# Optimization experiments

Measured on AMD Instinct MI355X. Metric: run time of the kernel, lower is better.

The kernel has to match this reference:

```python
import jax, jax.numpy as jnp
import numpy as np

NUM_TAGS = 5
START_TAG = 3  # ent_to_ix['<START>']
STOP_TAG = 4   # ent_to_ix['<STOP>']
NEG_INF = -10000.0
B, T = 8192, 512


def setup_inputs() -> dict:
    key = jax.random.key(0)
    k1, k2 = jax.random.split(key)
    feats = jax.random.normal(k1, (B, T, NUM_TAGS), dtype=jnp.float32)
    transitions = jax.random.normal(k2, (NUM_TAGS, NUM_TAGS), dtype=jnp.float32)
    # matches __init__: no transition into START, none out of STOP
    transitions = transitions.at[START_TAG, :].set(NEG_INF)
    transitions = transitions.at[:, STOP_TAG].set(NEG_INF)
    return {"feats": feats, "transitions": transitions}


def reference(feats, transitions):
    """Batched CRF forward algorithm (log partition function).

    feats: [B, T, K] emission scores; transitions: [K, K] where
    transitions[next, prev] is the score of prev -> next.
    Returns alpha: [B] log partition per sequence.
    """
    def single(seq):  # seq: [T, K]
        init = jnp.full((NUM_TAGS,), NEG_INF, dtype=seq.dtype).at[START_TAG].set(0.0)

        def step(forward_var, feat):
            # scores[next, prev] = forward_var[prev] + transitions[next, prev] + feat[next]
            scores = forward_var[None, :] + transitions + feat[:, None]
            return jax.nn.logsumexp(scores, axis=1), None

        forward_var, _ = jax.lax.scan(step, init, seq)
        terminal = forward_var + transitions[STOP_TAG]
        return jax.nn.logsumexp(terminal)

    return jax.vmap(single)(feats)
```

## Files before the change

### kernel.cpp

```cpp
#include <hip/hip_runtime.h>

#define BB 8192
#define SEQF 2560

__device__ __forceinline__ float rfl(float x) {
    return __int_as_float(__builtin_amdgcn_readfirstlane(__float_as_int(x)));
}

__global__ __launch_bounds__(256, 4) void crf_fused(const float* __restrict__ feats,
                                                    const float* __restrict__ trans,
                                                    float* __restrict__ out) {
    const int tid  = threadIdx.x;
    const int lane = tid & 63;
    const int gw   = blockIdx.x * 4 + (tid >> 6);
    const int s0   = gw * 2;

    const float4* pA = (const float4*)(feats + (size_t)s0 * SEQF) + lane * 10;
    const float4* pB = pA + (SEQF / 4);
    float4 a0=pA[0], a1=pA[1], a2=pA[2], a3=pA[3], a4=pA[4];
    float4 a5=pA[5], a6=pA[6], a7=pA[7], a8=pA[8], a9=pA[9];
    float4 b0=pB[0], b1=pB[1], b2=pB[2], b3=pB[3], b4=pB[4];
    float4 b5=pB[5], b6=pB[6], b7=pB[7], b8=pB[8], b9=pB[9];
    __builtin_amdgcn_sched_barrier(0);

    const float E00=rfl(__expf(trans[0])),  E01=rfl(__expf(trans[1])),  E02=rfl(__expf(trans[2]));
    const float E10=rfl(__expf(trans[5])),  E11=rfl(__expf(trans[6])),  E12=rfl(__expf(trans[7]));
    const float E20=rfl(__expf(trans[10])), E21=rfl(__expf(trans[11])), E22=rfl(__expf(trans[12]));
    const float C0 =rfl(__expf(trans[3])),  C1 =rfl(__expf(trans[8])),  C2 =rfl(__expf(trans[13]));
    const float S0 =rfl(__expf(trans[20])), S1 =rfl(__expf(trans[21])), S2 =rfl(__expf(trans[22]));

#define CRF_STEP(FA, FB, FC) do {                                   \
        float e0 = __expf(FA), e1 = __expf(FB), e2 = __expf(FC);    \
        float N00 = e0 * (E00*M00 + E01*M10 + E02*M20);             \
        float N01 = e0 * (E00*M01 + E01*M11 + E02*M21);             \
        float N02 = e0 * (E00*M02 + E01*M12 + E02*M22);             \
        float N10 = e1 * (E10*M00 + E11*M10 + E12*M20);             \
        float N11 = e1 * (E10*M01 + E11*M11 + E12*M21);             \
        float N12 = e1 * (E10*M02 + E11*M12 + E12*M22);             \
        float N20 = e2 * (E20*M00 + E21*M10 + E22*M20);             \
        float N21 = e2 * (E20*M01 + E21*M11 + E22*M21);             \
        float N22 = e2 * (E20*M02 + E21*M12 + E22*M22);             \
        M00=N00; M01=N01; M02=N02;                                  \
        M10=N10; M11=N11; M12=N12;                                  \
        M20=N20; M21=N21; M22=N22;                                  \
    } while (0)

#define CRF_RENORM() do {                                           \
        float mx = fmaxf(fmaxf(fmaxf(M00,M01), fmaxf(M02,M10)),     \
                         fmaxf(fmaxf(M11,M12), fmaxf(fmaxf(M20,M21),M22))); \
        mx = fmaxf(mx, 1e-30f);                                     \
        int ee = (int)((__float_as_uint(mx) >> 23) & 0xffu) - 127;  \
        float sc = __uint_as_float((unsigned)(127 - ee) << 23);     \
        ls += (float)ee;                                            \
        M00*=sc; M01*=sc; M02*=sc;                                  \
        M10*=sc; M11*=sc; M12*=sc;                                  \
        M20*=sc; M21*=sc; M22*=sc;                                  \
    } while (0)

#define TREE_LEVEL(D) do {                                          \
        float P00=__shfl_down(M00,D), P01=__shfl_down(M01,D), P02=__shfl_down(M02,D); \
        float P10=__shfl_down(M10,D), P11=__shfl_down(M11,D), P12=__shfl_down(M12,D); \
        float P20=__shfl_down(M20,D), P21=__shfl_down(M21,D), P22=__shfl_down(M22,D); \
        float Pls=__shfl_down(ls, D);                               \
        float N00 = P00*M00 + P01*M10 + P02*M20;                    \
        float N01 = P00*M01 + P01*M11 + P02*M21;                    \
        float N02 = P00*M02 + P01*M12 + P02*M22;                    \
        float N10 = P10*M00 + P11*M10 + P12*M20;                    \
        float N11 = P10*M01 + P11*M11 + P12*M21;                    \
        float N12 = P10*M02 + P11*M12 + P12*M22;                    \
        float N20 = P20*M00 + P21*M10 + P22*M20;                    \
        float N21 = P20*M01 + P21*M11 + P22*M21;                    \
        float N22 = P20*M02 + P21*M12 + P22*M22;                    \
        M00=N00; M01=N01; M02=N02; M10=N10; M11=N11; M12=N12;       \
        M20=N20; M21=N21; M22=N22;                                  \
        ls += Pls;                                                  \
        CRF_RENORM();                                               \
    } while (0)

#define CRF_SEQ(q0,q1,q2,q3,q4,q5,q6,q7,q8,q9, OUTIDX) do {         \
        float M00, M01, M02, M10, M11, M12, M20, M21, M22;          \
        float ls = 0.0f;                                            \
        {    \
            float e0 = __expf(q0.x), e1 = __expf(q0.y), e2 = __expf(q0.z); \
            M00 = e0*E00; M01 = e0*E01; M02 = e0*E02;               \
            M10 = e1*E10; M11 = e1*E11; M12 = e1*E12;               \
            M20 = e2*E20; M21 = e2*E21; M22 = e2*E22;               \
            if (lane == 0) {                                        \
                M00 = M01 = M02 = e0*C0;                            \
                M10 = M11 = M12 = e1*C1;                            \
                M20 = M21 = M22 = e2*C2;                            \
            }                                                       \
        }                                                           \
        CRF_STEP(q1.y, q1.z, q1.w);                         \
        CRF_STEP(q2.z, q2.w, q3.x);                         \
        CRF_STEP(q3.w, q4.x, q4.y);                         \
        CRF_RENORM();                                               \
        CRF_STEP(q5.x, q5.y, q5.z);                         \
        CRF_STEP(q6.y, q6.z, q6.w);                         \
        CRF_STEP(q7.z, q7.w, q8.x);                         \
        CRF_STEP(q8.w, q9.x, q9.y);                         \
        CRF_RENORM();                                               \
        TREE_LEVEL(1);  TREE_LEVEL(2);  TREE_LEVEL(4);              \
        TREE_LEVEL(8);  TREE_LEVEL(16); TREE_LEVEL(32);             \
        float r = S0*M00 + S1*M10 + S2*M20;                         \
        float res = __logf(r) + ls * 0.69314718055994531f;          \
        if (lane == 0) out[OUTIDX] = res;                           \
    } while (0)

    CRF_SEQ(a0,a1,a2,a3,a4,a5,a6,a7,a8,a9, s0);
    CRF_SEQ(b0,b1,b2,b3,b4,b5,b6,b7,b8,b9, s0 + 1);

#undef CRF_STEP
#undef CRF_RENORM
#undef TREE_LEVEL
#undef CRF_SEQ
}

extern "C" void kernel_launch(void* const* d_in, const int* in_sizes, int n_in,
                              void* d_out, int out_size, void* d_ws, size_t ws_size,
                              hipStream_t stream) {
    const float* feats = (const float*)d_in[0];
    const float* trans = (const float*)d_in[1];
    float* out = (float*)d_out;
    (void)d_ws; (void)ws_size;

    crf_fused<<<BB / 8, 256, 0, stream>>>(feats, trans, out);
}
```

Measured before the change: 20.95 us.

## Process two sequences per wavefront with 32-lane halves and longer chunks

```diff
diff --git a/kernel.cpp b/kernel.cpp
--- a/kernel.cpp
+++ b/kernel.cpp
@@ -12,15 +12,16 @@
                                                     float* __restrict__ out) {
     const int tid  = threadIdx.x;
     const int lane = tid & 63;
+    const int half = lane >> 5;
+    const int cpos = lane & 31;
     const int gw   = blockIdx.x * 4 + (tid >> 6);
     const int s0   = gw * 2;
 
-    const float4* pA = (const float4*)(feats + (size_t)s0 * SEQF) + lane * 10;
-    const float4* pB = pA + (SEQF / 4);
-    float4 a0=pA[0], a1=pA[1], a2=pA[2], a3=pA[3], a4=pA[4];
-    float4 a5=pA[5], a6=pA[6], a7=pA[7], a8=pA[8], a9=pA[9];
-    float4 b0=pB[0], b1=pB[1], b2=pB[2], b3=pB[3], b4=pB[4];
-    float4 b5=pB[5], b6=pB[6], b7=pB[7], b8=pB[8], b9=pB[9];
+    const float4* p = (const float4*)(feats + (size_t)(s0 + half) * SEQF) + cpos * 20;
+    float4 q0 =p[0],  q1 =p[1],  q2 =p[2],  q3 =p[3],  q4 =p[4];
+    float4 q5 =p[5],  q6 =p[6],  q7 =p[7],  q8 =p[8],  q9 =p[9];
+    float4 q10=p[10], q11=p[11], q12=p[12], q13=p[13], q14=p[14];
+    float4 q15=p[15], q16=p[16], q17=p[17], q18=p[18], q19=p[19];
     __builtin_amdgcn_sched_barrier(0);
 
     const float E00=rfl(__expf(trans[0])),  E01=rfl(__expf(trans[1])),  E02=rfl(__expf(trans[2]));
@@ -28,6 +29,11 @@
     const float E20=rfl(__expf(trans[10])), E21=rfl(__expf(trans[11])), E22=rfl(__expf(trans[12]));
     const float C0 =rfl(__expf(trans[3])),  C1 =rfl(__expf(trans[8])),  C2 =rfl(__expf(trans[13]));
     const float S0 =rfl(__expf(trans[20])), S1 =rfl(__expf(trans[21])), S2 =rfl(__expf(trans[22]));
+
+    const bool c0 = (cpos == 0);
+    const float G00 = c0 ? C0 : E00, G01 = c0 ? C0 : E01, G02 = c0 ? C0 : E02;
+    const float G10 = c0 ? C1 : E10, G11 = c0 ? C1 : E11, G12 = c0 ? C1 : E12;
+    const float G20 = c0 ? C2 : E20, G21 = c0 ? C2 : E21, G22 = c0 ? C2 : E22;
 
 #define CRF_STEP(FA, FB, FC) do {                                   \
         float e0 = __expf(FA), e1 = __expf(FB), e2 = __expf(FC);    \
@@ -57,7 +63,7 @@
         M20*=sc; M21*=sc; M22*=sc;                                  \
     } while (0)
 
-#define TREE_LEVEL(D) do {                                          \
+#define TREE_LEVEL(D, RN) do {                                      \
         float P00=__shfl_down(M00,D), P01=__shfl_down(M01,D), P02=__shfl_down(M02,D); \
         float P10=__shfl_down(M10,D), P11=__shfl_down(M11,D), P12=__shfl_down(M12,D); \
         float P20=__shfl_down(M20,D), P21=__shfl_down(M21,D), P22=__shfl_down(M22,D); \
@@ -74,46 +80,49 @@
         M00=N00; M01=N01; M02=N02; M10=N10; M11=N11; M12=N12;       \
         M20=N20; M21=N21; M22=N22;                                  \
         ls += Pls;                                                  \
-        CRF_RENORM();                                               \
+        if (RN) CRF_RENORM();                                       \
     } while (0)
 
-#define CRF_SEQ(q0,q1,q2,q3,q4,q5,q6,q7,q8,q9, OUTIDX) do {         \
-        float M00, M01, M02, M10, M11, M12, M20, M21, M22;          \
-        float ls = 0.0f;                                            \
-        {    \
-            float e0 = __expf(q0.x), e1 = __expf(q0.y), e2 = __expf(q0.z); \
-            M00 = e0*E00; M01 = e0*E01; M02 = e0*E02;               \
-            M10 = e1*E10; M11 = e1*E11; M12 = e1*E12;               \
-            M20 = e2*E20; M21 = e2*E21; M22 = e2*E22;               \
-            if (lane == 0) {                                        \
-                M00 = M01 = M02 = e0*C0;                            \
-                M10 = M11 = M12 = e1*C1;                            \
-                M20 = M21 = M22 = e2*C2;                            \
-            }                                                       \
-        }                                                           \
-        CRF_STEP(q1.y, q1.z, q1.w);                         \
-        CRF_STEP(q2.z, q2.w, q3.x);                         \
-        CRF_STEP(q3.w, q4.x, q4.y);                         \
-        CRF_RENORM();                                               \
-        CRF_STEP(q5.x, q5.y, q5.z);                         \
-        CRF_STEP(q6.y, q6.z, q6.w);                         \
-        CRF_STEP(q7.z, q7.w, q8.x);                         \
-        CRF_STEP(q8.w, q9.x, q9.y);                         \
-        CRF_RENORM();                                               \
-        TREE_LEVEL(1);  TREE_LEVEL(2);  TREE_LEVEL(4);              \
-        TREE_LEVEL(8);  TREE_LEVEL(16); TREE_LEVEL(32);             \
-        float r = S0*M00 + S1*M10 + S2*M20;                         \
-        float res = __logf(r) + ls * 0.69314718055994531f;          \
-        if (lane == 0) out[OUTIDX] = res;                           \
-    } while (0)
+    float M00, M01, M02, M10, M11, M12, M20, M21, M22;
+    float ls = 0.0f;
 
-    CRF_SEQ(a0,a1,a2,a3,a4,a5,a6,a7,a8,a9, s0);
-    CRF_SEQ(b0,b1,b2,b3,b4,b5,b6,b7,b8,b9, s0 + 1);
+    {
+        float e0 = __expf(q0.x), e1 = __expf(q0.y), e2 = __expf(q0.z);
+        M00 = e0*G00; M01 = e0*G01; M02 = e0*G02;
+        M10 = e1*G10; M11 = e1*G11; M12 = e1*G12;
+        M20 = e2*G20; M21 = e2*G21; M22 = e2*G22;
+    }
+    CRF_STEP(q1.y,  q1.z,  q1.w);
+    CRF_STEP(q2.z,  q2.w,  q3.x);
+    CRF_STEP(q3.w,  q4.x,  q4.y);
+    CRF_STEP(q5.x,  q5.y,  q5.z);
+    CRF_STEP(q6.y,  q6.z,  q6.w);
+    CRF_STEP(q7.z,  q7.w,  q8.x);
+    CRF_STEP(q8.w,  q9.x,  q9.y);
+    CRF_RENORM();
+    CRF_STEP(q10.x, q10.y, q10.z);
+    CRF_STEP(q11.y, q11.z, q11.w);
+    CRF_STEP(q12.z, q12.w, q13.x);
+    CRF_STEP(q13.w, q14.x, q14.y);
+    CRF_STEP(q15.x, q15.y, q15.z);
+    CRF_STEP(q16.y, q16.z, q16.w);
+    CRF_STEP(q17.z, q17.w, q18.x);
+    CRF_STEP(q18.w, q19.x, q19.y);
+    CRF_RENORM();
+
+    TREE_LEVEL(1, 0);
+    TREE_LEVEL(2, 1);
+    TREE_LEVEL(4, 0);
+    TREE_LEVEL(8, 1);
+    TREE_LEVEL(16, 1);
+
+    float r = S0*M00 + S1*M10 + S2*M20;
+    float res = __logf(r) + ls * 0.69314718055994531f;
+    if (cpos == 0) out[s0 + half] = res;
 
 #undef CRF_STEP
 #undef CRF_RENORM
 #undef TREE_LEVEL
-#undef CRF_SEQ
 }
 
 extern "C" void kernel_launch(void* const* d_in, const int* in_sizes, int n_in,
```

After: 19.60 us. 1.07x faster.
